# Optimization experiments

Hardware: AMD Instinct MI355X
Metric: run time of the kernel (lower is better)

Reference implementation:

```python
import jax, jax.numpy as jnp
import numpy as np
import math

B, S, D, H = 2, 2048, 512, 8
DH = D // H  # 64

def setup_inputs() -> dict:
    key = jax.random.key(0)
    ks = jax.random.split(key, 7)
    x = jax.random.normal(ks[0], (B, S, D), jnp.float32)
    shift = jax.random.normal(ks[1], (B, S, S), jnp.float32)
    mask = jax.random.randint(ks[2], (B, S, S), 0, 2).astype(jnp.float32)
    W = jax.random.normal(ks[3], (3 * D, D), jnp.float32) / math.sqrt(D)
    b = jnp.zeros((3 * D,), jnp.float32)
    Wo = jax.random.normal(ks[4], (D, D), jnp.float32) / math.sqrt(D)
    bo = jnp.zeros((D,), jnp.float32)
    return {"x": x, "shift": shift, "mask": mask, "W": W, "b": b, "Wo": Wo, "bo": bo}

def reference(x, shift, mask, W, b, Wo, bo):
    # qkv projection: (B,S,3D). torch chunk(n_heads) then chunk(3) =>
    # per-head layout is [q_h | k_h | v_h] within each 3*DH-sized slice.
    qkv = x @ W.T + b
    qkv = qkv.reshape(B, S, H, 3, DH)
    qkv = jnp.moveaxis(qkv, (2, 3), (0, 1))  # (H, 3, B, S, DH)
    q, k, v = qkv[:, 0], qkv[:, 1], qkv[:, 2]  # each (H, B, S, DH)

    head_scale = jnp.exp2(-jnp.arange(H, dtype=jnp.float32)).reshape(H, 1, 1, 1)  # 2^-h
    logits = jnp.einsum('hbqd,hbkd->hbqk', q, k) / math.sqrt(DH)
    logits = logits - head_scale * shift[None]          # ALiBi-style per-head shift
    m = mask[None]                                       # (1,B,S,S)
    logits = logits * m - 1e8 * (1.0 - m)
    att = jax.nn.softmax(logits, axis=-1)
    o = jnp.einsum('hbqk,hbkd->hbqd', att, v)            # (H,B,S,DH)
    o = jnp.moveaxis(o, 0, 2).reshape(B, S, D)           # concat heads on last dim
    return o @ Wo.T + bo
```

## Files before the change

### kernel.cpp

```cpp
#include <hip/hip_runtime.h>
#include <math.h>

constexpr int Bc = 2, Sc = 2048, Dc = 512, Hc = 8, DHc = 64;
constexpr int NQKV = 3 * Dc;

typedef unsigned short u16;
typedef unsigned int u32;
typedef __attribute__((ext_vector_type(8))) __bf16 bf16x8;
typedef __attribute__((ext_vector_type(16))) float f32x16;

#define MFMA32 __builtin_amdgcn_mfma_f32_32x32x16_bf16

__device__ inline uint2 splitpack2(float a, float b) {
  u32 ua = __float_as_uint(a), ub = __float_as_uint(b);
  u32 hi = (ub & 0xFFFF0000u) | (ua >> 16);
  float ra = a - __uint_as_float(ua & 0xFFFF0000u);
  float rb = b - __uint_as_float(ub & 0xFFFF0000u);
  u32 lo = (__float_as_uint(rb) & 0xFFFF0000u) | (__float_as_uint(ra) >> 16);
  return uint2{hi, lo};
}
__device__ inline void split1(float v, u16& hi, u16& lo) {
  u32 u = __float_as_uint(v);
  hi = (u16)(u >> 16);
  float r = v - __uint_as_float(u & 0xFFFF0000u);
  lo = (u16)(__float_as_uint(r) >> 16);
}

__global__ __launch_bounds__(256, 2) void gemm1_mfma(
    const float* __restrict__ x, const float* __restrict__ W,
    const float* __restrict__ bias, u16* __restrict__ Qhi,
    u16* __restrict__ Qlo, u16* __restrict__ Khi, u16* __restrict__ Klo,
    u16* __restrict__ Vthi, u16* __restrict__ Vtlo) {
  __shared__ __align__(16) u16 pool[18432];
  const int tid = threadIdx.x;
  const int wave = tid >> 6, lane = tid & 63, l31 = lane & 31, lhi = lane >> 5;
  const int wm = wave >> 1, wn = wave & 1;
  const int m0 = blockIdx.y * 128, n0 = blockIdx.x * 64;

  f32x16 acc[2];
#pragma unroll
  for (int r = 0; r < 16; ++r) {
    acc[0][r] = 0.f;
    acc[1][r] = 0.f;
  }

  for (int k0 = 0; k0 < 512; k0 += 32) {
#pragma unroll
    for (int i = 0; i < 2; ++i) {
      const int g = i * 256 + tid;
      const int m = g >> 2, kg = g & 3;
      const float* src = x + (size_t)(m0 + m) * 512 + k0 + kg * 8;
      const float4 v0 = *(const float4*)src;
      const float4 v1 = *(const float4*)(src + 4);
      const uint2 p0 = splitpack2(v0.x, v0.y), p1 = splitpack2(v0.z, v0.w);
      const uint2 p2 = splitpack2(v1.x, v1.y), p3 = splitpack2(v1.z, v1.w);
      const int row = (kg & 1) * 32 + (m & 31);
      *(uint4*)&pool[((((0 * 4 + (m >> 5)) * 2 + (kg >> 1)) * 64 + row)) * 8] =
          uint4{p0.x, p1.x, p2.x, p3.x};
      *(uint4*)&pool[((((1 * 4 + (m >> 5)) * 2 + (kg >> 1)) * 64 + row)) * 8] =
          uint4{p0.y, p1.y, p2.y, p3.y};
    }
    {
      const int n = tid >> 2, kg = tid & 3;
      const float* src = W + (size_t)(n0 + n) * 512 + k0 + kg * 8;
      const float4 v0 = *(const float4*)src;
      const float4 v1 = *(const float4*)(src + 4);
      const uint2 p0 = splitpack2(v0.x, v0.y), p1 = splitpack2(v0.z, v0.w);
      const uint2 p2 = splitpack2(v1.x, v1.y), p3 = splitpack2(v1.z, v1.w);
      const int row = (kg & 1) * 32 + (n & 31);
      *(uint4*)&pool[8192 +
                     ((((0 * 2 + (n >> 5)) * 2 + (kg >> 1)) * 64 + row)) * 8] =
          uint4{p0.x, p1.x, p2.x, p3.x};
      *(uint4*)&pool[8192 +
                     ((((1 * 2 + (n >> 5)) * 2 + (kg >> 1)) * 64 + row)) * 8] =
          uint4{p0.y, p1.y, p2.y, p3.y};
    }
    __syncthreads();
#pragma unroll
    for (int t = 0; t < 2; ++t) {
      const bf16x8 bh =
          *(const bf16x8*)&pool[8192 + (((0 * 2 + wn) * 2 + t) * 64 + lane) * 8];
      const bf16x8 bl =
          *(const bf16x8*)&pool[8192 + (((1 * 2 + wn) * 2 + t) * 64 + lane) * 8];
#pragma unroll
      for (int ti = 0; ti < 2; ++ti) {
        const bf16x8 ah =
            *(const bf16x8*)&pool[(((0 * 4 + wm * 2 + ti) * 2 + t) * 64 + lane) * 8];
        const bf16x8 al =
            *(const bf16x8*)&pool[(((1 * 4 + wm * 2 + ti) * 2 + t) * 64 + lane) * 8];
        acc[ti] = MFMA32(ah, bh, acc[ti], 0, 0, 0);
        acc[ti] = MFMA32(ah, bl, acc[ti], 0, 0, 0);
        acc[ti] = MFMA32(al, bh, acc[ti], 0, 0, 0);
      }
    }
    __syncthreads();
  }

  const int n = n0 + wn * 32 + l31;
  const float bn = bias[n];
  const int h = n0 / 192;
  const int t3 = (n0 % 192) / 64;
  const int dh = wn * 32 + l31;
  const int batch = m0 >> 11;
  const int s0 = m0 & 2047;
  const int hbq = h * 2 + batch;

#pragma unroll
  for (int ti = 0; ti < 2; ++ti)
#pragma unroll
    for (int r = 0; r < 16; ++r) {
      const int tl = wm * 64 + ti * 32 + (r & 3) + 8 * (r >> 2) + 4 * lhi;
      float val = acc[ti][r] + bn;
      if (t3 == 0) val *= 0.125f;
      u16 hi, lo;
      split1(val, hi, lo);
      pool[tl * 72 + dh] = hi;
      pool[9216 + tl * 72 + dh] = lo;
    }
  __syncthreads();

  u16 *d0, *d1;
  if (t3 == 0) {
    d0 = Qhi;
    d1 = Qlo;
  } else if (t3 == 1) {
    d0 = Khi;
    d1 = Klo;
  } else {
    d0 = Vthi;
    d1 = Vtlo;
  }

  if (t3 != 2) {
    const size_t base = ((size_t)hbq * 2048 + s0) * 64;
#pragma unroll
    for (int p = 0; p < 2; ++p) {
      u16* dst = (p ? d1 : d0) + base;
#pragma unroll
      for (int j = 0; j < 4; ++j) {
        const int g = tid * 32 + j * 8;
        const int token = g >> 6, dh8 = g & 63;
        *(uint4*)(dst + g) = *(const uint4*)&pool[p * 9216 + token * 72 + dh8];
      }
    }
  } else {
    const int d = tid >> 2, tp = (tid & 3) * 32;
#pragma unroll
    for (int p = 0; p < 2; ++p) {
      u16* dst = (p ? d1 : d0) + ((size_t)hbq * 64 + d) * 2048 + s0 + tp;
      u32 w[16];
#pragma unroll
      for (int j = 0; j < 16; ++j) {
        const u16 a = pool[p * 9216 + (tp + 2 * j) * 72 + d];
        const u16 b2 = pool[p * 9216 + (tp + 2 * j + 1) * 72 + d];
        w[j] = (u32)a | ((u32)b2 << 16);
      }
#pragma unroll
      for (int j = 0; j < 4; ++j)
        *(uint4*)(dst + j * 8) =
            uint4{w[4 * j], w[4 * j + 1], w[4 * j + 2], w[4 * j + 3]};
    }
  }
}

constexpr int KF0 = 8320;
constexpr int VF0 = 24704;
constexpr int PF0 = 41088;

__global__ __launch_bounds__(512, 1) void attn_mfma(
    const u16* __restrict__ Qhi, const u16* __restrict__ Qlo,
    const u16* __restrict__ Khi, const u16* __restrict__ Klo,
    const u16* __restrict__ Vthi, const u16* __restrict__ Vtlo,
    const float* __restrict__ shift, const float* __restrict__ mask,
    u16* __restrict__ Othi, u16* __restrict__ Otlo) {
  const int hp = blockIdx.z, b = blockIdx.y, qb = blockIdx.x;
  const int tid = threadIdx.x;
  const int wave = tid >> 6;
  const int hsel = wave >> 2, wq = (wave >> 1) & 1, wk = wave & 1;
  const int lane = tid & 63;
  const int l31 = lane & 31, lhi = lane >> 5;

  __shared__ __align__(16) u16 smem[57472];
  float* SMs = (float*)smem;
  u16* Pw = smem + PF0 + wave * 2048;

  const int head = hp * 2 + hsel;
  const size_t hb = (size_t)head * Bc + b;
  const int ql = wq * 32 + l31;
  const int qg = qb * 64 + ql;

  bf16x8 qf[2][4];
  {
    const size_t qbase = (hb * Sc + qg) * DHc;
#pragma unroll
    for (int t = 0; t < 4; ++t) {
      qf[0][t] = *(const bf16x8*)(Qhi + qbase + t * 16 + lhi * 8);
      qf[1][t] = *(const bf16x8*)(Qlo + qbase + t * 16 + lhi * 8);
    }
  }
  const float hs = exp2f(-(float)head);

  const int smq = tid >> 3, smk = (tid & 7) * 8;
  const float* shr = shift + ((size_t)b * Sc + qb * 64 + smq) * Sc + smk;
  const float* mkr = mask + ((size_t)b * Sc + qb * 64 + smq) * Sc + smk;

  const int kr = lane >> 1, kh2 = lane & 1;
  const size_t kfix = (hb * Sc + wk * 32 + kr) * 64 + kh2 * 32;
  const size_t vfix = (hb * 64 + lane) * 2048 + wk * 32;
  const int vmt = lane >> 5, vdl = lane & 31;

  float m_run = -INFINITY, l_run = 0.f;
  f32x16 o0, o1;
#pragma unroll
  for (int i = 0; i < 16; ++i) {
    o0[i] = 0.f;
    o1[i] = 0.f;
  }

  for (int it = 0; it < 32; ++it) {
    const int kt = it * 64;
    {
      const float4 s0 = *(const float4*)(shr + kt);
      const float4 s1 = *(const float4*)(shr + kt + 4);
      const float4 m0 = *(const float4*)(mkr + kt);
      const float4 m1 = *(const float4*)(mkr + kt + 4);
      float* dst = SMs + (size_t)smk * 65 + smq;
      dst[0 * 65] = (m0.x != 0.f) ? s0.x : 1e13f;
      dst[1 * 65] = (m0.y != 0.f) ? s0.y : 1e13f;
      dst[2 * 65] = (m0.z != 0.f) ? s0.z : 1e13f;
      dst[3 * 65] = (m0.w != 0.f) ? s0.w : 1e13f;
      dst[4 * 65] = (m1.x != 0.f) ? s1.x : 1e13f;
      dst[5 * 65] = (m1.y != 0.f) ? s1.y : 1e13f;
      dst[6 * 65] = (m1.z != 0.f) ? s1.z : 1e13f;
      dst[7 * 65] = (m1.w != 0.f) ? s1.w : 1e13f;
    }
    if (wq == 0) {
      const size_t gb = kfix + (size_t)kt * 64;
#pragma unroll
      for (int c = 0; c < 4; ++c) {
        const int dhc = kh2 * 32 + c * 8;
        const int t = dhc >> 4, lh = (dhc >> 3) & 1;
        *(uint4*)&smem[KF0 + ((((hsel * 2 + 0) * 2 + wk) * 4 + t) * 64 +
                              lh * 32 + kr) * 8] =
            *(const uint4*)(Khi + gb + c * 8);
        *(uint4*)&smem[KF0 + ((((hsel * 2 + 1) * 2 + wk) * 4 + t) * 64 +
                              lh * 32 + kr) * 8] =
            *(const uint4*)(Klo + gb + c * 8);
      }
    } else {
      const size_t gb = vfix + kt;
#pragma unroll
      for (int c = 0; c < 4; ++c) {
        const int t = c >> 1, lh = c & 1;
        *(uint4*)&smem[VF0 + (((((hsel * 2 + 0) * 2 + wk) * 2 + vmt) * 2 + t) *
                                  64 + lh * 32 + vdl) * 8] =
            *(const uint4*)(Vthi + gb + c * 8);
        *(uint4*)&smem[VF0 + (((((hsel * 2 + 1) * 2 + wk) * 2 + vmt) * 2 + t) *
                                  64 + lh * 32 + vdl) * 8] =
            *(const uint4*)(Vtlo + gb + c * 8);
      }
    }
    __syncthreads();

    f32x16 s;
#pragma unroll
    for (int i = 0; i < 16; ++i) s[i] = 0.f;
#pragma unroll
    for (int t = 0; t < 4; ++t) {
      const bf16x8 kh = *(const bf16x8*)&smem[KF0 +
          ((((hsel * 2 + 0) * 2 + wk) * 4 + t) * 64 + lane) * 8];
      const bf16x8 kl = *(const bf16x8*)&smem[KF0 +
          ((((hsel * 2 + 1) * 2 + wk) * 4 + t) * 64 + lane) * 8];
      s = MFMA32(kh, qf[0][t], s, 0, 0, 0);
      s = MFMA32(kh, qf[1][t], s, 0, 0, 0);
      s = MFMA32(kl, qf[0][t], s, 0, 0, 0);
    }

    float p[16];
    float kmax = -INFINITY;
#pragma unroll
    for (int c = 0; c < 4; ++c) {
#pragma unroll
      for (int e = 0; e < 4; ++e) {
        const int kl_ = wk * 32 + c * 8 + lhi * 4 + e;
        const float a = hs * SMs[(size_t)kl_ * 65 + ql];
        const float lg = s[4 * c + e] - a;
        p[4 * c + e] = lg;
        kmax = fmaxf(kmax, lg);
      }
    }
    kmax = fmaxf(kmax, __shfl_xor(kmax, 32, 64));
    const float mnew = fmaxf(m_run, kmax);
    const float alpha = __expf(m_run - mnew);
    float rsum = 0.f;
#pragma unroll
    for (int r = 0; r < 16; ++r) {
      p[r] = __expf(p[r] - mnew);
      rsum += p[r];
    }
    rsum += __shfl_xor(rsum, 32, 64);
    l_run = l_run * alpha + rsum;
    m_run = mnew;
#pragma unroll
    for (int i = 0; i < 16; ++i) {
      o0[i] *= alpha;
      o1[i] *= alpha;
    }

#pragma unroll
    for (int c = 0; c < 4; ++c) {
      const uint2 s01 = splitpack2(p[4 * c + 0], p[4 * c + 1]);
      const uint2 s23 = splitpack2(p[4 * c + 2], p[4 * c + 3]);
      const int t = c >> 1, lh = c & 1;
      const int bi = (t * 64 + lh * 32 + l31) * 8 + lhi * 4;
      *(uint2*)&Pw[bi] = uint2{s01.x, s23.x};
      *(uint2*)&Pw[1024 + bi] = uint2{s01.y, s23.y};
    }

#pragma unroll
    for (int t = 0; t < 2; ++t) {
      const bf16x8 ph = *(const bf16x8*)&Pw[(t * 64 + lane) * 8];
      const bf16x8 pl_ = *(const bf16x8*)&Pw[1024 + (t * 64 + lane) * 8];
      bf16x8 vh = *(const bf16x8*)&smem[VF0 +
          (((((hsel * 2 + 0) * 2 + wk) * 2 + 0) * 2 + t) * 64 + lane) * 8];
      bf16x8 vl = *(const bf16x8*)&smem[VF0 +
          (((((hsel * 2 + 1) * 2 + wk) * 2 + 0) * 2 + t) * 64 + lane) * 8];
      o0 = MFMA32(vh, ph, o0, 0, 0, 0);
      o0 = MFMA32(vh, pl_, o0, 0, 0, 0);
      o0 = MFMA32(vl, ph, o0, 0, 0, 0);
      vh = *(const bf16x8*)&smem[VF0 +
          (((((hsel * 2 + 0) * 2 + wk) * 2 + 1) * 2 + t) * 64 + lane) * 8];
      vl = *(const bf16x8*)&smem[VF0 +
          (((((hsel * 2 + 1) * 2 + wk) * 2 + 1) * 2 + t) * 64 + lane) * 8];
      o1 = MFMA32(vh, ph, o1, 0, 0, 0);
      o1 = MFMA32(vh, pl_, o1, 0, 0, 0);
      o1 = MFMA32(vl, ph, o1, 0, 0, 0);
    }
    __syncthreads();
  }

  float* mL = (float*)(smem + KF0);
  float* lL = mL + 128;
  float* Om = lL + 128;
  if (wk == 1) {
    if (lhi == 0) {
      mL[(hsel * 2 + wq) * 32 + l31] = m_run;
      lL[(hsel * 2 + wq) * 32 + l31] = l_run;
    }
#pragma unroll
    for (int mt = 0; mt < 2; ++mt)
#pragma unroll
      for (int r = 0; r < 16; ++r) {
        const int row = mt * 32 + (r & 3) + 8 * (r >> 2) + 4 * lhi;
        Om[((hsel * 2 + wq) * 64 + row) * 33 + l31] = (mt ? o1[r] : o0[r]);
      }
  }
  __syncthreads();
  if (wk == 0) {
    const float m1 = mL[(hsel * 2 + wq) * 32 + l31];
    const float l1v = lL[(hsel * 2 + wq) * 32 + l31];
    const float mst = fmaxf(m_run, m1);
    const float a0 = __expf(m_run - mst), a1 = __expf(m1 - mst);
    const float inv = 1.f / (a0 * l_run + a1 * l1v);
    const int tok = b * 2048 + qg;
#pragma unroll
    for (int mt = 0; mt < 2; ++mt)
#pragma unroll
      for (int r = 0; r < 16; ++r) {
        const int row = mt * 32 + (r & 3) + 8 * (r >> 2) + 4 * lhi;
        const float val = (a0 * (mt ? o1[r] : o0[r]) +
                           a1 * Om[((hsel * 2 + wq) * 64 + row) * 33 + l31]) *
                          inv;
        const int d = head * 64 + row;
        u16 hi, lo;
        split1(val, hi, lo);
        const size_t idx = ((size_t)(d >> 3) * 4096 + tok) * 8 + (d & 7);
        Othi[idx] = hi;
        Otlo[idx] = lo;
      }
  }
}

__global__ __launch_bounds__(256, 2) void gemm2_mfma(
    const u16* __restrict__ Othi, const u16* __restrict__ Otlo,
    const float* __restrict__ Wo, const float* __restrict__ bo,
    float* __restrict__ out) {
  __shared__ __align__(16) u16 Af[2][2][2][64][8];
  __shared__ __align__(16) u16 Bf[2][2][2][64][8];
  const int tid = threadIdx.x;
  const int wave = tid >> 6, lane = tid & 63, l31 = lane & 31, lhi = lane >> 5;
  const int wm = wave >> 1, wn = wave & 1;
  const int m0 = blockIdx.y * 64, n0 = blockIdx.x * 64;

  f32x16 acc;
#pragma unroll
  for (int r = 0; r < 16; ++r) acc[r] = 0.f;

  for (int k0 = 0; k0 < 512; k0 += 32) {
#pragma unroll
    for (int i = 0; i < 2; ++i) {
      const int f = i * 256 + tid;
      const int p = f >> 8, rem = f & 255, c = rem >> 6, tok = rem & 63;
      const u16* src =
          (p ? Otlo : Othi) + ((size_t)(k0 / 8 + c) * 4096 + m0 + tok) * 8;
      *(uint4*)&Af[p][tok >> 5][c >> 1][(c & 1) * 32 + (tok & 31)][0] =
          *(const uint4*)src;
    }
    {
      const int n = tid >> 2, c = tid & 3;
      const float* src = Wo + (size_t)(n0 + n) * 512 + k0 + c * 8;
      const float4 v0 = *(const float4*)src;
      const float4 v1 = *(const float4*)(src + 4);
      const uint2 q0 = splitpack2(v0.x, v0.y), q1 = splitpack2(v0.z, v0.w);
      const uint2 q2 = splitpack2(v1.x, v1.y), q3 = splitpack2(v1.z, v1.w);
      *(uint4*)&Bf[0][n >> 5][c >> 1][(c & 1) * 32 + (n & 31)][0] =
          uint4{q0.x, q1.x, q2.x, q3.x};
      *(uint4*)&Bf[1][n >> 5][c >> 1][(c & 1) * 32 + (n & 31)][0] =
          uint4{q0.y, q1.y, q2.y, q3.y};
    }
    __syncthreads();
#pragma unroll
    for (int t = 0; t < 2; ++t) {
      const bf16x8 ah = *(const bf16x8*)&Af[0][wm][t][lane][0];
      const bf16x8 al = *(const bf16x8*)&Af[1][wm][t][lane][0];
      const bf16x8 bh = *(const bf16x8*)&Bf[0][wn][t][lane][0];
      const bf16x8 bl = *(const bf16x8*)&Bf[1][wn][t][lane][0];
      acc = MFMA32(ah, bh, acc, 0, 0, 0);
      acc = MFMA32(ah, bl, acc, 0, 0, 0);
      acc = MFMA32(al, bh, acc, 0, 0, 0);
    }
    __syncthreads();
  }

  const int n = n0 + wn * 32 + l31;
  const float bn = bo[n];
#pragma unroll
  for (int r = 0; r < 16; ++r) {
    const int m = m0 + wm * 32 + (r & 3) + 8 * (r >> 2) + 4 * lhi;
    out[(size_t)m * 512 + n] = acc[r] + bn;
  }
}

extern "C" void kernel_launch(void* const* d_in, const int* in_sizes, int n_in,
                              void* d_out, int out_size, void* d_ws,
                              size_t ws_size, hipStream_t stream) {
  const float* x = (const float*)d_in[0];
  const float* shift = (const float*)d_in[1];
  const float* mask = (const float*)d_in[2];
  const float* W = (const float*)d_in[3];
  const float* b = (const float*)d_in[4];
  const float* Wo = (const float*)d_in[5];
  const float* bo = (const float*)d_in[6];
  float* out = (float*)d_out;

  const size_t P = (size_t)Hc * Bc * Sc * DHc;
  u16* ws0 = (u16*)d_ws;
  u16* Qhi = ws0;
  u16* Qlo = ws0 + P;
  u16* Khi = ws0 + 2 * P;
  u16* Klo = ws0 + 3 * P;
  u16* Vthi = ws0 + 4 * P;
  u16* Vtlo = ws0 + 5 * P;
  u16* Othi = ws0 + 6 * P;
  u16* Otlo = ws0 + 7 * P;

  gemm1_mfma<<<dim3(NQKV / 64, (Bc * Sc) / 128), 256, 0, stream>>>(
      x, W, b, Qhi, Qlo, Khi, Klo, Vthi, Vtlo);

  attn_mfma<<<dim3(Sc / 64, Bc, Hc / 2), 512, 0, stream>>>(
      Qhi, Qlo, Khi, Klo, Vthi, Vtlo, shift, mask, Othi, Otlo);

  gemm2_mfma<<<dim3(Dc / 64, (Bc * Sc) / 64), 256, 0, stream>>>(Othi, Otlo, Wo,
                                                                bo, out);
}
```

Measured before the change: 286.1 us.

## Enlarge attention tile to 128 queries, pass P via shuffles, remap grid

The attention kernel now runs 1024-thread blocks, each covering 128 queries per head pair. This halves how often the K/V tiles are staged per query and lets the shift/mask tile be shared across more waves. The P operand for the PV MFMA is now built in registers with cross-half lane shuffles instead of a per-wave LDS round trip, and the shift/mask LDS tile is transposed to row-major. A 1D grid interleaves head pairs and batches so that neighbouring blocks read the same shift/mask rows. In exchange the grid shrinks to 128 blocks, which lowers occupancy and parallelism, and the larger blocks may raise register pressure.

```diff
diff --git a/kernel.cpp b/kernel.cpp
--- a/kernel.cpp
+++ b/kernel.cpp
@@ -25,6 +25,11 @@
   float r = v - __uint_as_float(u & 0xFFFF0000u);
   lo = (u16)(__float_as_uint(r) >> 16);
 }
+
+union U8 {
+  uint4 u;
+  bf16x8 v;
+};
 
 __global__ __launch_bounds__(256, 2) void gemm1_mfma(
     const float* __restrict__ x, const float* __restrict__ W,
@@ -163,31 +168,32 @@
   }
 }
 
-constexpr int KF0 = 8320;
-constexpr int VF0 = 24704;
-constexpr int PF0 = 41088;
-
-__global__ __launch_bounds__(512, 1) void attn_mfma(
+constexpr int KF0 = 16640;
+constexpr int VF0 = 33024;
+
+__global__ __launch_bounds__(1024, 1) void attn_mfma(
     const u16* __restrict__ Qhi, const u16* __restrict__ Qlo,
     const u16* __restrict__ Khi, const u16* __restrict__ Klo,
     const u16* __restrict__ Vthi, const u16* __restrict__ Vtlo,
     const float* __restrict__ shift, const float* __restrict__ mask,
     u16* __restrict__ Othi, u16* __restrict__ Otlo) {
-  const int hp = blockIdx.z, b = blockIdx.y, qb = blockIdx.x;
+  const int bid = blockIdx.x;
+  const int comb = bid & 7;
+  const int hp = comb >> 1, b = comb & 1;
+  const int qb = bid >> 3;
   const int tid = threadIdx.x;
   const int wave = tid >> 6;
-  const int hsel = wave >> 2, wq = (wave >> 1) & 1, wk = wave & 1;
+  const int hsel = wave >> 3, wq = (wave >> 1) & 3, wk = wave & 1;
   const int lane = tid & 63;
   const int l31 = lane & 31, lhi = lane >> 5;
 
-  __shared__ __align__(16) u16 smem[57472];
+  __shared__ __align__(16) u16 smem[49408];
   float* SMs = (float*)smem;
-  u16* Pw = smem + PF0 + wave * 2048;
 
   const int head = hp * 2 + hsel;
   const size_t hb = (size_t)head * Bc + b;
   const int ql = wq * 32 + l31;
-  const int qg = qb * 64 + ql;
+  const int qg = qb * 128 + ql;
 
   bf16x8 qf[2][4];
   {
@@ -201,8 +207,8 @@
   const float hs = exp2f(-(float)head);
 
   const int smq = tid >> 3, smk = (tid & 7) * 8;
-  const float* shr = shift + ((size_t)b * Sc + qb * 64 + smq) * Sc + smk;
-  const float* mkr = mask + ((size_t)b * Sc + qb * 64 + smq) * Sc + smk;
+  const float* shr = shift + ((size_t)b * Sc + qb * 128 + smq) * Sc + smk;
+  const float* mkr = mask + ((size_t)b * Sc + qb * 128 + smq) * Sc + smk;
 
   const int kr = lane >> 1, kh2 = lane & 1;
   const size_t kfix = (hb * Sc + wk * 32 + kr) * 64 + kh2 * 32;
@@ -224,15 +230,15 @@
       const float4 s1 = *(const float4*)(shr + kt + 4);
       const float4 m0 = *(const float4*)(mkr + kt);
       const float4 m1 = *(const float4*)(mkr + kt + 4);
-      float* dst = SMs + (size_t)smk * 65 + smq;
-      dst[0 * 65] = (m0.x != 0.f) ? s0.x : 1e13f;
-      dst[1 * 65] = (m0.y != 0.f) ? s0.y : 1e13f;
-      dst[2 * 65] = (m0.z != 0.f) ? s0.z : 1e13f;
-      dst[3 * 65] = (m0.w != 0.f) ? s0.w : 1e13f;
-      dst[4 * 65] = (m1.x != 0.f) ? s1.x : 1e13f;
-      dst[5 * 65] = (m1.y != 0.f) ? s1.y : 1e13f;
-      dst[6 * 65] = (m1.z != 0.f) ? s1.z : 1e13f;
-      dst[7 * 65] = (m1.w != 0.f) ? s1.w : 1e13f;
+      float* dst = SMs + (size_t)smq * 65 + smk;
+      dst[0] = (m0.x != 0.f) ? s0.x : 1e13f;
+      dst[1] = (m0.y != 0.f) ? s0.y : 1e13f;
+      dst[2] = (m0.z != 0.f) ? s0.z : 1e13f;
+      dst[3] = (m0.w != 0.f) ? s0.w : 1e13f;
+      dst[4] = (m1.x != 0.f) ? s1.x : 1e13f;
+      dst[5] = (m1.y != 0.f) ? s1.y : 1e13f;
+      dst[6] = (m1.z != 0.f) ? s1.z : 1e13f;
+      dst[7] = (m1.w != 0.f) ? s1.w : 1e13f;
     }
     if (wq == 0) {
       const size_t gb = kfix + (size_t)kt * 64;
@@ -247,7 +253,7 @@
                               lh * 32 + kr) * 8] =
             *(const uint4*)(Klo + gb + c * 8);
       }
-    } else {
+    } else if (wq == 1) {
       const size_t gb = vfix + kt;
 #pragma unroll
       for (int c = 0; c < 4; ++c) {
@@ -283,7 +289,7 @@
 #pragma unroll
       for (int e = 0; e < 4; ++e) {
         const int kl_ = wk * 32 + c * 8 + lhi * 4 + e;
-        const float a = hs * SMs[(size_t)kl_ * 65 + ql];
+        const float a = hs * SMs[(size_t)ql * 65 + kl_];
         const float lg = s[4 * c + e] - a;
         p[4 * c + e] = lg;
         kmax = fmaxf(kmax, lg);
@@ -307,58 +313,65 @@
       o1[i] *= alpha;
     }
 
-#pragma unroll
-    for (int c = 0; c < 4; ++c) {
-      const uint2 s01 = splitpack2(p[4 * c + 0], p[4 * c + 1]);
-      const uint2 s23 = splitpack2(p[4 * c + 2], p[4 * c + 3]);
-      const int t = c >> 1, lh = c & 1;
-      const int bi = (t * 64 + lh * 32 + l31) * 8 + lhi * 4;
-      *(uint2*)&Pw[bi] = uint2{s01.x, s23.x};
-      *(uint2*)&Pw[1024 + bi] = uint2{s01.y, s23.y};
-    }
+    float oth[16];
+#pragma unroll
+    for (int r = 0; r < 16; ++r) oth[r] = __shfl_xor(p[r], 32, 64);
 
 #pragma unroll
     for (int t = 0; t < 2; ++t) {
-      const bf16x8 ph = *(const bf16x8*)&Pw[(t * 64 + lane) * 8];
-      const bf16x8 pl_ = *(const bf16x8*)&Pw[1024 + (t * 64 + lane) * 8];
+      float f[8];
+#pragma unroll
+      for (int j = 0; j < 4; ++j) {
+        f[j] = lhi ? oth[t * 8 + 4 + j] : p[t * 8 + j];
+        f[4 + j] = lhi ? p[t * 8 + 4 + j] : oth[t * 8 + j];
+      }
+      const uint2 a01 = splitpack2(f[0], f[1]);
+      const uint2 a23 = splitpack2(f[2], f[3]);
+      const uint2 a45 = splitpack2(f[4], f[5]);
+      const uint2 a67 = splitpack2(f[6], f[7]);
+      U8 Phi, Plo;
+      Phi.u = uint4{a01.x, a23.x, a45.x, a67.x};
+      Plo.u = uint4{a01.y, a23.y, a45.y, a67.y};
+
       bf16x8 vh = *(const bf16x8*)&smem[VF0 +
           (((((hsel * 2 + 0) * 2 + wk) * 2 + 0) * 2 + t) * 64 + lane) * 8];
       bf16x8 vl = *(const bf16x8*)&smem[VF0 +
           (((((hsel * 2 + 1) * 2 + wk) * 2 + 0) * 2 + t) * 64 + lane) * 8];
-      o0 = MFMA32(vh, ph, o0, 0, 0, 0);
-      o0 = MFMA32(vh, pl_, o0, 0, 0, 0);
-      o0 = MFMA32(vl, ph, o0, 0, 0, 0);
+      o0 = MFMA32(vh, Phi.v, o0, 0, 0, 0);
+      o0 = MFMA32(vh, Plo.v, o0, 0, 0, 0);
+      o0 = MFMA32(vl, Phi.v, o0, 0, 0, 0);
       vh = *(const bf16x8*)&smem[VF0 +
           (((((hsel * 2 + 0) * 2 + wk) * 2 + 1) * 2 + t) * 64 + lane) * 8];
       vl = *(const bf16x8*)&smem[VF0 +
           (((((hsel * 2 + 1) * 2 + wk) * 2 + 1) * 2 + t) * 64 + lane) * 8];
-      o1 = MFMA32(vh, ph, o1, 0, 0, 0);
-      o1 = MFMA32(vh, pl_, o1, 0, 0, 0);
-      o1 = MFMA32(vl, ph, o1, 0, 0, 0);
-    }
-    __syncthreads();
-  }
-
-  float* mL = (float*)(smem + KF0);
-  float* lL = mL + 128;
-  float* Om = lL + 128;
+      o1 = MFMA32(vh, Phi.v, o1, 0, 0, 0);
+      o1 = MFMA32(vh, Plo.v, o1, 0, 0, 0);
+      o1 = MFMA32(vl, Phi.v, o1, 0, 0, 0);
+    }
+    __syncthreads();
+  }
+
+  float* mL = (float*)smem;
+  float* lL = mL + 256;
+  float* Om = lL + 256;
+  const int pair = hsel * 4 + wq;
   if (wk == 1) {
     if (lhi == 0) {
-      mL[(hsel * 2 + wq) * 32 + l31] = m_run;
-      lL[(hsel * 2 + wq) * 32 + l31] = l_run;
+      mL[pair * 32 + l31] = m_run;
+      lL[pair * 32 + l31] = l_run;
     }
 #pragma unroll
     for (int mt = 0; mt < 2; ++mt)
 #pragma unroll
       for (int r = 0; r < 16; ++r) {
         const int row = mt * 32 + (r & 3) + 8 * (r >> 2) + 4 * lhi;
-        Om[((hsel * 2 + wq) * 64 + row) * 33 + l31] = (mt ? o1[r] : o0[r]);
+        Om[(pair * 64 + row) * 33 + l31] = (mt ? o1[r] : o0[r]);
       }
   }
   __syncthreads();
   if (wk == 0) {
-    const float m1 = mL[(hsel * 2 + wq) * 32 + l31];
-    const float l1v = lL[(hsel * 2 + wq) * 32 + l31];
+    const float m1 = mL[pair * 32 + l31];
+    const float l1v = lL[pair * 32 + l31];
     const float mst = fmaxf(m_run, m1);
     const float a0 = __expf(m_run - mst), a1 = __expf(m1 - mst);
     const float inv = 1.f / (a0 * l_run + a1 * l1v);
@@ -368,9 +381,9 @@
 #pragma unroll
       for (int r = 0; r < 16; ++r) {
         const int row = mt * 32 + (r & 3) + 8 * (r >> 2) + 4 * lhi;
-        const float val = (a0 * (mt ? o1[r] : o0[r]) +
-                           a1 * Om[((hsel * 2 + wq) * 64 + row) * 33 + l31]) *
-                          inv;
+        const float val =
+            (a0 * (mt ? o1[r] : o0[r]) + a1 * Om[(pair * 64 + row) * 33 + l31]) *
+            inv;
         const int d = head * 64 + row;
         u16 hi, lo;
         split1(val, hi, lo);
@@ -467,8 +480,8 @@
   gemm1_mfma<<<dim3(NQKV / 64, (Bc * Sc) / 128), 256, 0, stream>>>(
       x, W, b, Qhi, Qlo, Khi, Klo, Vthi, Vtlo);
 
-  attn_mfma<<<dim3(Sc / 64, Bc, Hc / 2), 512, 0, stream>>>(
-      Qhi, Qlo, Khi, Klo, Vthi, Vtlo, shift, mask, Othi, Otlo);
+  attn_mfma<<<128, 1024, 0, stream>>>(Qhi, Qlo, Khi, Klo, Vthi, Vtlo, shift,
+                                      mask, Othi, Otlo);
 
   gemm2_mfma<<<dim3(Dc / 64, (Bc * Sc) / 64), 256, 0, stream>>>(Othi, Otlo, Wo,
                                                                 bo, out);
```

Measured after the change: 358.8 us. 1.25x slower.

## Pre-split inputs to bf16 hi/lo and widen QKV GEMM tile to 128x128

Applied to the files above, without the earlier changes.

Adds a separate kernel that splits x and W into bf16 hi/lo arrays once, stored in scratch (x in the output buffer, W in the O workspace region that is overwritten later). The QKV GEMM then loads pre-split bf16 directly, and its N tile doubles to 128, so each wave computes a 2x2 grid of MFMA tiles and reuses each loaded fragment across more MFMAs. This removes the per-block repeated float-to-bf16 splitting and halves how often x is reloaded. In exchange it adds an extra launch and global round-trip for the split data, and the epilogue now runs two serialized passes through shared memory.

```diff
diff --git a/kernel.cpp b/kernel.cpp
--- a/kernel.cpp
+++ b/kernel.cpp
@@ -26,8 +26,31 @@
   lo = (u16)(__float_as_uint(r) >> 16);
 }
 
+constexpr int NX4 = (4096 * 512) / 4;
+constexpr int NW4 = (1536 * 512) / 4;
+
+__global__ __launch_bounds__(256) void split_inputs(
+    const float* __restrict__ x, const float* __restrict__ W,
+    u16* __restrict__ xhi, u16* __restrict__ xlo, u16* __restrict__ whi,
+    u16* __restrict__ wlo) {
+  const int f = blockIdx.x * 256 + threadIdx.x;
+  const float* src;
+  u16 *dh_, *dl_;
+  int idx;
+  if (f < NX4) {
+    src = x; dh_ = xhi; dl_ = xlo; idx = f;
+  } else {
+    src = W; dh_ = whi; dl_ = wlo; idx = f - NX4;
+  }
+  const float4 v = ((const float4*)src)[idx];
+  const uint2 p0 = splitpack2(v.x, v.y), p1 = splitpack2(v.z, v.w);
+  ((uint2*)dh_)[idx] = uint2{p0.x, p1.x};
+  ((uint2*)dl_)[idx] = uint2{p0.y, p1.y};
+}
+
 __global__ __launch_bounds__(256, 2) void gemm1_mfma(
-    const float* __restrict__ x, const float* __restrict__ W,
+    const u16* __restrict__ xhi, const u16* __restrict__ xlo,
+    const u16* __restrict__ whi, const u16* __restrict__ wlo,
     const float* __restrict__ bias, u16* __restrict__ Qhi,
     u16* __restrict__ Qlo, u16* __restrict__ Khi, u16* __restrict__ Klo,
     u16* __restrict__ Vthi, u16* __restrict__ Vtlo) {
@@ -35,130 +58,134 @@
   const int tid = threadIdx.x;
   const int wave = tid >> 6, lane = tid & 63, l31 = lane & 31, lhi = lane >> 5;
   const int wm = wave >> 1, wn = wave & 1;
-  const int m0 = blockIdx.y * 128, n0 = blockIdx.x * 64;
-
-  f32x16 acc[2];
-#pragma unroll
-  for (int r = 0; r < 16; ++r) {
-    acc[0][r] = 0.f;
-    acc[1][r] = 0.f;
-  }
+  const int m0 = blockIdx.y * 128, n0 = blockIdx.x * 128;
+
+  f32x16 acc[2][2];
+#pragma unroll
+  for (int mi = 0; mi < 2; ++mi)
+#pragma unroll
+    for (int nj = 0; nj < 2; ++nj)
+#pragma unroll
+      for (int r = 0; r < 16; ++r) acc[mi][nj][r] = 0.f;
 
   for (int k0 = 0; k0 < 512; k0 += 32) {
 #pragma unroll
-    for (int i = 0; i < 2; ++i) {
+    for (int i = 0; i < 4; ++i) {
       const int g = i * 256 + tid;
-      const int m = g >> 2, kg = g & 3;
-      const float* src = x + (size_t)(m0 + m) * 512 + k0 + kg * 8;
-      const float4 v0 = *(const float4*)src;
-      const float4 v1 = *(const float4*)(src + 4);
-      const uint2 p0 = splitpack2(v0.x, v0.y), p1 = splitpack2(v0.z, v0.w);
-      const uint2 p2 = splitpack2(v1.x, v1.y), p3 = splitpack2(v1.z, v1.w);
-      const int row = (kg & 1) * 32 + (m & 31);
-      *(uint4*)&pool[((((0 * 4 + (m >> 5)) * 2 + (kg >> 1)) * 64 + row)) * 8] =
-          uint4{p0.x, p1.x, p2.x, p3.x};
-      *(uint4*)&pool[((((1 * 4 + (m >> 5)) * 2 + (kg >> 1)) * 64 + row)) * 8] =
-          uint4{p0.y, p1.y, p2.y, p3.y};
-    }
-    {
-      const int n = tid >> 2, kg = tid & 3;
-      const float* src = W + (size_t)(n0 + n) * 512 + k0 + kg * 8;
-      const float4 v0 = *(const float4*)src;
-      const float4 v1 = *(const float4*)(src + 4);
-      const uint2 p0 = splitpack2(v0.x, v0.y), p1 = splitpack2(v0.z, v0.w);
-      const uint2 p2 = splitpack2(v1.x, v1.y), p3 = splitpack2(v1.z, v1.w);
-      const int row = (kg & 1) * 32 + (n & 31);
-      *(uint4*)&pool[8192 +
-                     ((((0 * 2 + (n >> 5)) * 2 + (kg >> 1)) * 64 + row)) * 8] =
-          uint4{p0.x, p1.x, p2.x, p3.x};
-      *(uint4*)&pool[8192 +
-                     ((((1 * 2 + (n >> 5)) * 2 + (kg >> 1)) * 64 + row)) * 8] =
-          uint4{p0.y, p1.y, p2.y, p3.y};
+      const int p = g >> 9, rem = g & 511, m = rem >> 2, c = rem & 3;
+      const u16* src = (p ? xlo : xhi) + (size_t)(m0 + m) * 512 + k0 + c * 8;
+      *(uint4*)&pool[(((p * 4 + (m >> 5)) * 2 + (c >> 1)) * 64 +
+                      (c & 1) * 32 + (m & 31)) * 8] = *(const uint4*)src;
+    }
+#pragma unroll
+    for (int i = 0; i < 4; ++i) {
+      const int g = i * 256 + tid;
+      const int p = g >> 9, rem = g & 511, n = rem >> 2, c = rem & 3;
+      const u16* src = (p ? wlo : whi) + (size_t)(n0 + n) * 512 + k0 + c * 8;
+      *(uint4*)&pool[8192 + (((p * 4 + (n >> 5)) * 2 + (c >> 1)) * 64 +
+                             (c & 1) * 32 + (n & 31)) * 8] = *(const uint4*)src;
     }
     __syncthreads();
 #pragma unroll
     for (int t = 0; t < 2; ++t) {
-      const bf16x8 bh =
-          *(const bf16x8*)&pool[8192 + (((0 * 2 + wn) * 2 + t) * 64 + lane) * 8];
-      const bf16x8 bl =
-          *(const bf16x8*)&pool[8192 + (((1 * 2 + wn) * 2 + t) * 64 + lane) * 8];
-#pragma unroll
-      for (int ti = 0; ti < 2; ++ti) {
-        const bf16x8 ah =
-            *(const bf16x8*)&pool[(((0 * 4 + wm * 2 + ti) * 2 + t) * 64 + lane) * 8];
-        const bf16x8 al =
-            *(const bf16x8*)&pool[(((1 * 4 + wm * 2 + ti) * 2 + t) * 64 + lane) * 8];
-        acc[ti] = MFMA32(ah, bh, acc[ti], 0, 0, 0);
-        acc[ti] = MFMA32(ah, bl, acc[ti], 0, 0, 0);
-        acc[ti] = MFMA32(al, bh, acc[ti], 0, 0, 0);
-      }
-    }
-    __syncthreads();
-  }
-
-  const int n = n0 + wn * 32 + l31;
-  const float bn = bias[n];
-  const int h = n0 / 192;
-  const int t3 = (n0 % 192) / 64;
-  const int dh = wn * 32 + l31;
-  const int batch = m0 >> 11;
-  const int s0 = m0 & 2047;
-  const int hbq = h * 2 + batch;
-
-#pragma unroll
-  for (int ti = 0; ti < 2; ++ti)
-#pragma unroll
-    for (int r = 0; r < 16; ++r) {
-      const int tl = wm * 64 + ti * 32 + (r & 3) + 8 * (r >> 2) + 4 * lhi;
-      float val = acc[ti][r] + bn;
-      if (t3 == 0) val *= 0.125f;
-      u16 hi, lo;
-      split1(val, hi, lo);
-      pool[tl * 72 + dh] = hi;
-      pool[9216 + tl * 72 + dh] = lo;
-    }
-  __syncthreads();
-
-  u16 *d0, *d1;
-  if (t3 == 0) {
-    d0 = Qhi;
-    d1 = Qlo;
-  } else if (t3 == 1) {
-    d0 = Khi;
-    d1 = Klo;
-  } else {
-    d0 = Vthi;
-    d1 = Vtlo;
-  }
-
-  if (t3 != 2) {
-    const size_t base = ((size_t)hbq * 2048 + s0) * 64;
-#pragma unroll
-    for (int p = 0; p < 2; ++p) {
-      u16* dst = (p ? d1 : d0) + base;
-#pragma unroll
-      for (int j = 0; j < 4; ++j) {
-        const int g = tid * 32 + j * 8;
-        const int token = g >> 6, dh8 = g & 63;
-        *(uint4*)(dst + g) = *(const uint4*)&pool[p * 9216 + token * 72 + dh8];
-      }
-    }
-  } else {
-    const int d = tid >> 2, tp = (tid & 3) * 32;
-#pragma unroll
-    for (int p = 0; p < 2; ++p) {
-      u16* dst = (p ? d1 : d0) + ((size_t)hbq * 64 + d) * 2048 + s0 + tp;
-      u32 w[16];
-#pragma unroll
-      for (int j = 0; j < 16; ++j) {
-        const u16 a = pool[p * 9216 + (tp + 2 * j) * 72 + d];
-        const u16 b2 = pool[p * 9216 + (tp + 2 * j + 1) * 72 + d];
-        w[j] = (u32)a | ((u32)b2 << 16);
-      }
-#pragma unroll
-      for (int j = 0; j < 4; ++j)
-        *(uint4*)(dst + j * 8) =
-            uint4{w[4 * j], w[4 * j + 1], w[4 * j + 2], w[4 * j + 3]};
+      bf16x8 bh[2], bl[2], ah[2], al[2];
+#pragma unroll
+      for (int nj = 0; nj < 2; ++nj) {
+        const int nt = wn * 2 + nj;
+        bh[nj] = *(const bf16x8*)&pool[8192 +
+                                       (((0 * 4 + nt) * 2 + t) * 64 + lane) * 8];
+        bl[nj] = *(const bf16x8*)&pool[8192 +
+                                       (((1 * 4 + nt) * 2 + t) * 64 + lane) * 8];
+      }
+#pragma unroll
+      for (int mi = 0; mi < 2; ++mi) {
+        const int mt = wm * 2 + mi;
+        ah[mi] = *(const bf16x8*)&pool[(((0 * 4 + mt) * 2 + t) * 64 + lane) * 8];
+        al[mi] = *(const bf16x8*)&pool[(((1 * 4 + mt) * 2 + t) * 64 + lane) * 8];
+      }
+#pragma unroll
+      for (int mi = 0; mi < 2; ++mi)
+#pragma unroll
+        for (int nj = 0; nj < 2; ++nj) {
+          acc[mi][nj] = MFMA32(ah[mi], bh[nj], acc[mi][nj], 0, 0, 0);
+          acc[mi][nj] = MFMA32(ah[mi], bl[nj], acc[mi][nj], 0, 0, 0);
+          acc[mi][nj] = MFMA32(al[mi], bh[nj], acc[mi][nj], 0, 0, 0);
+        }
+    }
+    __syncthreads();
+  }
+
+  const int batch = m0 >> 11, s0 = m0 & 2047;
+#pragma unroll
+  for (int hn = 0; hn < 2; ++hn) {
+    const int nh0 = n0 + hn * 64;
+    const int h = nh0 / 192, t3 = (nh0 % 192) / 64;
+    const int hbq = h * 2 + batch;
+    __syncthreads();
+    if (wn == hn) {
+#pragma unroll
+      for (int nj = 0; nj < 2; ++nj) {
+        const float bn = bias[nh0 + nj * 32 + l31];
+        const int dh = nj * 32 + l31;
+#pragma unroll
+        for (int mi = 0; mi < 2; ++mi)
+#pragma unroll
+          for (int r = 0; r < 16; ++r) {
+            const int tl =
+                (wm * 2 + mi) * 32 + (r & 3) + 8 * (r >> 2) + 4 * lhi;
+            float val = acc[mi][nj][r] + bn;
+            if (t3 == 0) val *= 0.125f;
+            u16 hi, lo;
+            split1(val, hi, lo);
+            pool[tl * 72 + dh] = hi;
+            pool[9216 + tl * 72 + dh] = lo;
+          }
+      }
+    }
+    __syncthreads();
+
+    u16 *d0, *d1;
+    if (t3 == 0) {
+      d0 = Qhi;
+      d1 = Qlo;
+    } else if (t3 == 1) {
+      d0 = Khi;
+      d1 = Klo;
+    } else {
+      d0 = Vthi;
+      d1 = Vtlo;
+    }
+
+    if (t3 != 2) {
+      const size_t base = ((size_t)hbq * 2048 + s0) * 64;
+#pragma unroll
+      for (int p = 0; p < 2; ++p) {
+        u16* dst = (p ? d1 : d0) + base;
+#pragma unroll
+        for (int j = 0; j < 4; ++j) {
+          const int g = tid * 32 + j * 8;
+          const int token = g >> 6, dh8 = g & 63;
+          *(uint4*)(dst + g) =
+              *(const uint4*)&pool[p * 9216 + token * 72 + dh8];
+        }
+      }
+    } else {
+      const int d = tid >> 2, tp = (tid & 3) * 32;
+#pragma unroll
+      for (int p = 0; p < 2; ++p) {
+        u16* dst = (p ? d1 : d0) + ((size_t)hbq * 64 + d) * 2048 + s0 + tp;
+        u32 w[16];
+#pragma unroll
+        for (int j = 0; j < 16; ++j) {
+          const u16 a = pool[p * 9216 + (tp + 2 * j) * 72 + d];
+          const u16 b2 = pool[p * 9216 + (tp + 2 * j + 1) * 72 + d];
+          w[j] = (u32)a | ((u32)b2 << 16);
+        }
+#pragma unroll
+        for (int j = 0; j < 4; ++j)
+          *(uint4*)(dst + j * 8) =
+              uint4{w[4 * j], w[4 * j + 1], w[4 * j + 2], w[4 * j + 3]};
+      }
     }
   }
 }
@@ -461,11 +488,18 @@
   u16* Klo = ws0 + 3 * P;
   u16* Vthi = ws0 + 4 * P;
   u16* Vtlo = ws0 + 5 * P;
+  u16* Whi = ws0 + 6 * P;
+  u16* Wlo = Whi + (size_t)NQKV * Dc;
   u16* Othi = ws0 + 6 * P;
   u16* Otlo = ws0 + 7 * P;
-
-  gemm1_mfma<<<dim3(NQKV / 64, (Bc * Sc) / 128), 256, 0, stream>>>(
-      x, W, b, Qhi, Qlo, Khi, Klo, Vthi, Vtlo);
+  u16* xhi = (u16*)d_out;
+  u16* xlo = xhi + P;
+
+  split_inputs<<<(NX4 + NW4) / 256, 256, 0, stream>>>(x, W, xhi, xlo, Whi,
+                                                      Wlo);
+
+  gemm1_mfma<<<dim3(NQKV / 128, (Bc * Sc) / 128), 256, 0, stream>>>(
+      xhi, xlo, Whi, Wlo, b, Qhi, Qlo, Khi, Klo, Vthi, Vtlo);
 
   attn_mfma<<<dim3(Sc / 64, Bc, Hc / 2), 512, 0, stream>>>(
       Qhi, Qlo, Khi, Klo, Vthi, Vtlo, shift, mask, Othi, Otlo);
```

Measured after the change: 292.1 us. 2.1% more time.
